# Kernel tuning notes

Hardware: AMD Instinct MI355X
Metric: run time of the kernel (lower is better)

The kernel has to match this reference:

```python
import jax, jax.numpy as jnp
import numpy as np

N = 8192
E = 262144
DIN = 512
DOUT = 256


def setup_inputs() -> dict:
    key = jax.random.key(0)
    k1, k2, k3, k4 = jax.random.split(key, 4)
    x = jax.random.normal(k1, (N, DIN), dtype=jnp.float32)
    edge_index = jax.random.randint(k2, (2, E), 0, N, dtype=jnp.int64)
    edge_weight = jax.random.uniform(k3, (E,), dtype=jnp.float32)
    W = jax.random.normal(k4, (DOUT, DIN), dtype=jnp.float32) * (1.0 / np.sqrt(DIN))
    return {"x": x, "edge_index": edge_index, "edge_weight": edge_weight, "W": W}


def reference(x, edge_index, edge_weight, W):
    n = x.shape[0]
    # Linear(dim_in, dim_out, bias=False): h = x @ W.T  -> [N, DOUT]
    h = x @ W.T
    # Dense adjacency: A[src, dst] += w (to_dense_adj sums duplicate edges)
    src, dst = edge_index[0], edge_index[1]
    A = jnp.zeros((n, n), dtype=x.dtype).at[src, dst].add(edge_weight)
    # degree from A BEFORE self-loops, then +1 from the added eye on degree_matrix
    deg = jnp.sum(A, axis=1) + 1.0
    # sqrt(inverse(diag(deg))) == diag(1/sqrt(deg)); apply as row scaling
    dinv_sqrt = 1.0 / jnp.sqrt(deg)  # [N]
    A = A + jnp.eye(n, dtype=x.dtype)  # self-loops on adjacency
    # x = D^{-1/2} @ (A.T @ (D^{-1/2} @ h))
    h = dinv_sqrt[:, None] * h
    h = A.T @ h
    h = dinv_sqrt[:, None] * h
    return h
```

## Files before the change

### kernel.cpp

```cpp
#include <hip/hip_runtime.h>

static constexpr int DIN = 512;
static constexpr int DOUT = 256;
static constexpr int CAP = 128;

typedef __attribute__((ext_vector_type(8))) short short8;
typedef __attribute__((ext_vector_type(4))) float f32x4;
typedef __attribute__((ext_vector_type(2))) unsigned int u32x2;
typedef __attribute__((ext_vector_type(4))) unsigned int u32x4;

__device__ inline unsigned short f2bf(float f) {
  unsigned int b = __float_as_uint(f);
  unsigned int r = (b + 0x7fffu + ((b >> 16) & 1u)) >> 16;
  return (unsigned short)r;
}
__device__ inline float bf_lo(unsigned int packed) { return __uint_as_float(packed << 16); }
__device__ inline float bf_hi(unsigned int packed) { return __uint_as_float(packed & 0xffff0000u); }

__device__ inline short8 cvt8(const f32x4 a, const f32x4 b) {
  short8 o;
  o[0] = (short)f2bf(a[0]); o[1] = (short)f2bf(a[1]);
  o[2] = (short)f2bf(a[2]); o[3] = (short)f2bf(a[3]);
  o[4] = (short)f2bf(b[0]); o[5] = (short)f2bf(b[1]);
  o[6] = (short)f2bf(b[2]); o[7] = (short)f2bf(b[3]);
  return o;
}

__global__ __launch_bounds__(256) void k_prep(
    const float* __restrict__ W, unsigned short* __restrict__ wbb,
    int* __restrict__ dz, int n2, int wgroups) {
  const int gid = blockIdx.x * 256 + threadIdx.x;
  if (gid < n2) dz[gid] = 0;
  const int wi = gid - n2;
  if (wi >= 0 && wi < wgroups) {
    const f32x4* src = (const f32x4*)(W + (size_t)wi * 8);
    f32x4 a = src[0], b = src[1];
    *(short8*)(wbb + (size_t)wi * 8) = cvt8(a, b);
  }
}

__global__ __launch_bounds__(256) void k_fused(
    const int* __restrict__ ei, const float* __restrict__ ew,
    const float* __restrict__ x, const unsigned short* __restrict__ wbb,
    float* __restrict__ deg, int* __restrict__ cursor,
    uint2* __restrict__ bucket, unsigned short* __restrict__ h1b, int E) {
  {
    const int e = blockIdx.x * 256 + threadIdx.x;
    if (e < E) {
      int srcv = __builtin_nontemporal_load(ei + e);
      int dstv = __builtin_nontemporal_load(ei + E + e);
      float w = __builtin_nontemporal_load(ew + e);
      atomicAdd(&deg[srcv], w);
      int pos = atomicAdd(&cursor[dstv], 1);
      if (pos < CAP) {
        uint2 v;
        v.x = (unsigned)srcv;
        v.y = __float_as_uint(w);
        bucket[(size_t)dstv * CAP + pos] = v;
      }
    }
  }
  const int lane = threadIdx.x & 63;
  const int wv = threadIdx.x >> 6;
  const int bm = (blockIdx.x >> 1) * 16;
  const int colb = (blockIdx.x & 1) * 128 + wv * 32;
  const int r = lane & 15;
  const int kg = lane >> 4;
  f32x4 acc[2] = {};
  const float* arow = x + (size_t)(bm + r) * DIN + kg * 8;
  const unsigned short* brow = wbb + (size_t)(colb + r) * DIN + kg * 8;
#pragma unroll
  for (int k0 = 0; k0 < DIN; k0 += 32) {
    f32x4 a0 = *(const f32x4*)(arow + k0);
    f32x4 a1 = *(const f32x4*)(arow + k0 + 4);
    short8 av = cvt8(a0, a1);
    short8 b0 = *(const short8*)(brow + k0);
    short8 b1 = *(const short8*)(brow + (size_t)16 * DIN + k0);
    acc[0] = __builtin_amdgcn_mfma_f32_16x16x32_bf16(av, b0, acc[0], 0, 0, 0);
    acc[1] = __builtin_amdgcn_mfma_f32_16x16x32_bf16(av, b1, acc[1], 0, 0, 0);
  }
#pragma unroll
  for (int i = 0; i < 4; ++i) {
    int row = bm + kg * 4 + i;
    h1b[(size_t)row * DOUT + colb + r] = f2bf(acc[0][i]);
    h1b[(size_t)row * DOUT + colb + 16 + r] = f2bf(acc[1][i]);
  }
}

__global__ __launch_bounds__(256, 4) void k_gather(
    const unsigned short* __restrict__ h1b, const float* __restrict__ deg,
    const int* __restrict__ cursor, const uint2* __restrict__ bucket,
    float* __restrict__ out) {
  const int lane = threadIdx.x & 63;
  const int wv = threadIdx.x >> 6;
  const int dst = blockIdx.x * 4 + wv;
  const int cl = lane & 31;
  const int half = lane >> 5;
  const int cnt = min(cursor[dst], CAP);

  const u32x4 selfv = *(const u32x4*)(h1b + (size_t)dst * DOUT + cl * 8);
  const float sd = __frsqrt_rn(1.0f + deg[dst]);

  float acc[8] = {};

  for (int base = 0; base < cnt; base += 64) {
    const int c = min(64, cnt - base);
    int sv = 0;
    float wl = 0.f;
    if (lane < c) {
      u32x2 ev = __builtin_nontemporal_load(
          (const u32x2*)(bucket + (size_t)dst * CAP + base + lane));
      sv = (int)ev[0];
      wl = __uint_as_float(ev[1]) * __frsqrt_rn(1.0f + deg[sv]);
    }
    const int npair = ((c + 15) >> 4) << 3;
    for (int j = 0; j < npair; j += 8) {
      u32x4 rbuf[8];
#pragma unroll
      for (int u = 0; u < 8; ++u) {
        int src = __shfl(sv, 2 * (j + u) + half);
        rbuf[u] = *(const u32x4*)(h1b + (size_t)src * DOUT + cl * 8);
      }
#pragma unroll
      for (int u = 0; u < 8; ++u) {
        float w = __shfl(wl, 2 * (j + u) + half);
        acc[0] = fmaf(w, bf_lo(rbuf[u][0]), acc[0]);
        acc[1] = fmaf(w, bf_hi(rbuf[u][0]), acc[1]);
        acc[2] = fmaf(w, bf_lo(rbuf[u][1]), acc[2]);
        acc[3] = fmaf(w, bf_hi(rbuf[u][1]), acc[3]);
        acc[4] = fmaf(w, bf_lo(rbuf[u][2]), acc[4]);
        acc[5] = fmaf(w, bf_hi(rbuf[u][2]), acc[5]);
        acc[6] = fmaf(w, bf_lo(rbuf[u][3]), acc[6]);
        acc[7] = fmaf(w, bf_hi(rbuf[u][3]), acc[7]);
      }
    }
  }

#pragma unroll
  for (int k = 0; k < 8; ++k) acc[k] += __shfl_xor(acc[k], 32);

  if (half == 0) {
    f32x4 o0v, o1v;
    o0v[0] = sd * fmaf(sd, bf_lo(selfv[0]), acc[0]);
    o0v[1] = sd * fmaf(sd, bf_hi(selfv[0]), acc[1]);
    o0v[2] = sd * fmaf(sd, bf_lo(selfv[1]), acc[2]);
    o0v[3] = sd * fmaf(sd, bf_hi(selfv[1]), acc[3]);
    o1v[0] = sd * fmaf(sd, bf_lo(selfv[2]), acc[4]);
    o1v[1] = sd * fmaf(sd, bf_hi(selfv[2]), acc[5]);
    o1v[2] = sd * fmaf(sd, bf_lo(selfv[3]), acc[6]);
    o1v[3] = sd * fmaf(sd, bf_hi(selfv[3]), acc[7]);
    float* op = out + (size_t)dst * DOUT + cl * 8;
    __builtin_nontemporal_store(o0v, (f32x4*)op);
    __builtin_nontemporal_store(o1v, (f32x4*)(op + 4));
  }
}

extern "C" void kernel_launch(void* const* d_in, const int* in_sizes, int n_in,
                              void* d_out, int out_size, void* d_ws, size_t ws_size,
                              hipStream_t stream) {
  const float* x = (const float*)d_in[0];
  const int* ei = (const int*)d_in[1];
  const float* ew = (const float*)d_in[2];
  const float* W = (const float*)d_in[3];
  float* out = (float*)d_out;

  const int n = in_sizes[0] / DIN;
  const int E = in_sizes[2];

  char* p = (char*)d_ws;
  auto alloc = [&](size_t bytes) {
    char* q = p;
    p += (bytes + 255) & ~(size_t)255;
    return q;
  };
  unsigned short* h1b = (unsigned short*)alloc((size_t)n * DOUT * 2);
  unsigned short* wbb = (unsigned short*)alloc((size_t)DOUT * DIN * 2);
  float* deg   = (float*)alloc((size_t)n * 4 * 2);
  int* cursor  = (int*)(deg + n);
  uint2* bucket = (uint2*)alloc((size_t)n * CAP * 8);

  const int n2 = 2 * n;
  const int wgroups = DOUT * DIN / 8;
  const int prep_blocks = (n2 + wgroups + 255) / 256;

  k_prep<<<prep_blocks, 256, 0, stream>>>(W, wbb, (int*)deg, n2, wgroups);
  k_fused<<<(E + 255) / 256, 256, 0, stream>>>(ei, ew, x, wbb, deg, cursor,
                                               bucket, h1b, E);
  k_gather<<<n / 4, 256, 0, stream>>>(h1b, deg, cursor, bucket, out);
}
```

Baseline: 73.34 us.

## Split fused kernel into separate edge-scatter and GEMM block roles

Each block of the fused kernel used to do one edge scatter per thread and then a 16x128 GEMM tile. Now blocks are assigned one role only: edge blocks handle 8 edges per thread with their atomics batched, and GEMM blocks compute a full 16x256 tile with 4 MFMA accumulators per wave. This cuts the grid size, amortises index loads, and reuses each x row across all output columns, so x is read only once. The risk is load imbalance between the two block types, and E must be divisible by 2048 because there is no tail handling.

```diff
diff --git a/kernel.cpp b/kernel.cpp
--- a/kernel.cpp
+++ b/kernel.cpp
@@ -3,6 +3,7 @@
 static constexpr int DIN = 512;
 static constexpr int DOUT = 256;
 static constexpr int CAP = 128;
+static constexpr int EPT = 8;
 
 typedef __attribute__((ext_vector_type(8))) short short8;
 typedef __attribute__((ext_vector_type(4))) float f32x4;
@@ -39,51 +40,68 @@
   }
 }
 
-__global__ __launch_bounds__(256) void k_fused(
+__global__ __launch_bounds__(256) void k_work(
     const int* __restrict__ ei, const float* __restrict__ ew,
     const float* __restrict__ x, const unsigned short* __restrict__ wbb,
     float* __restrict__ deg, int* __restrict__ cursor,
-    uint2* __restrict__ bucket, unsigned short* __restrict__ h1b, int E) {
-  {
-    const int e = blockIdx.x * 256 + threadIdx.x;
-    if (e < E) {
-      int srcv = __builtin_nontemporal_load(ei + e);
-      int dstv = __builtin_nontemporal_load(ei + E + e);
-      float w = __builtin_nontemporal_load(ew + e);
-      atomicAdd(&deg[srcv], w);
-      int pos = atomicAdd(&cursor[dstv], 1);
-      if (pos < CAP) {
+    uint2* __restrict__ bucket, unsigned short* __restrict__ h1b,
+    int E, int EBLK) {
+  const int b = blockIdx.x;
+  if (b < EBLK) {
+    const int e0 = b * 256 * EPT + threadIdx.x;
+    int sv[EPT], dv[EPT];
+    float wv[EPT];
+#pragma unroll
+    for (int u = 0; u < EPT; ++u) {
+      const int e = e0 + u * 256;
+      sv[u] = __builtin_nontemporal_load(ei + e);
+      dv[u] = __builtin_nontemporal_load(ei + E + e);
+      wv[u] = __builtin_nontemporal_load(ew + e);
+    }
+    int pos[EPT];
+#pragma unroll
+    for (int u = 0; u < EPT; ++u) pos[u] = atomicAdd(&cursor[dv[u]], 1);
+#pragma unroll
+    for (int u = 0; u < EPT; ++u) atomicAdd(&deg[sv[u]], wv[u]);
+#pragma unroll
+    for (int u = 0; u < EPT; ++u) {
+      if (pos[u] < CAP) {
         uint2 v;
-        v.x = (unsigned)srcv;
-        v.y = __float_as_uint(w);
-        bucket[(size_t)dstv * CAP + pos] = v;
+        v.x = (unsigned)sv[u];
+        v.y = __float_as_uint(wv[u]);
+        bucket[(size_t)dv[u] * CAP + pos[u]] = v;
       }
     }
-  }
+    return;
+  }
+  const int g = b - EBLK;
   const int lane = threadIdx.x & 63;
   const int wv = threadIdx.x >> 6;
-  const int bm = (blockIdx.x >> 1) * 16;
-  const int colb = (blockIdx.x & 1) * 128 + wv * 32;
+  const int bm = g * 16;
+  const int colb = wv * 64;
   const int r = lane & 15;
   const int kg = lane >> 4;
-  f32x4 acc[2] = {};
+  f32x4 acc[4] = {};
   const float* arow = x + (size_t)(bm + r) * DIN + kg * 8;
-  const unsigned short* brow = wbb + (size_t)(colb + r) * DIN + kg * 8;
+  const unsigned short* brow0 = wbb + (size_t)(colb + r) * DIN + kg * 8;
 #pragma unroll
   for (int k0 = 0; k0 < DIN; k0 += 32) {
     f32x4 a0 = *(const f32x4*)(arow + k0);
     f32x4 a1 = *(const f32x4*)(arow + k0 + 4);
     short8 av = cvt8(a0, a1);
-    short8 b0 = *(const short8*)(brow + k0);
-    short8 b1 = *(const short8*)(brow + (size_t)16 * DIN + k0);
-    acc[0] = __builtin_amdgcn_mfma_f32_16x16x32_bf16(av, b0, acc[0], 0, 0, 0);
-    acc[1] = __builtin_amdgcn_mfma_f32_16x16x32_bf16(av, b1, acc[1], 0, 0, 0);
+#pragma unroll
+    for (int nt = 0; nt < 4; ++nt) {
+      short8 bv = *(const short8*)(brow0 + (size_t)nt * 16 * DIN + k0);
+      acc[nt] = __builtin_amdgcn_mfma_f32_16x16x32_bf16(av, bv, acc[nt], 0, 0, 0);
+    }
   }
 #pragma unroll
   for (int i = 0; i < 4; ++i) {
     int row = bm + kg * 4 + i;
-    h1b[(size_t)row * DOUT + colb + r] = f2bf(acc[0][i]);
-    h1b[(size_t)row * DOUT + colb + 16 + r] = f2bf(acc[1][i]);
+#pragma unroll
+    for (int nt = 0; nt < 4; ++nt) {
+      h1b[(size_t)row * DOUT + colb + nt * 16 + r] = f2bf(acc[nt][i]);
+    }
   }
 }
 
@@ -183,8 +201,11 @@
   const int wgroups = DOUT * DIN / 8;
   const int prep_blocks = (n2 + wgroups + 255) / 256;
 
+  const int EBLK = E / (256 * EPT);
+  const int GB = n / 16;
+
   k_prep<<<prep_blocks, 256, 0, stream>>>(W, wbb, (int*)deg, n2, wgroups);
-  k_fused<<<(E + 255) / 256, 256, 0, stream>>>(ei, ew, x, wbb, deg, cursor,
-                                               bucket, h1b, E);
+  k_work<<<EBLK + GB, 256, 0, stream>>>(ei, ew, x, wbb, deg, cursor, bucket,
+                                        h1b, E, EBLK);
   k_gather<<<n / 4, 256, 0, stream>>>(h1b, deg, cursor, bucket, out);
 }
```

After: 70.78 us. 1.04x faster.
